# Kernel optimization log

Hardware: AMD Instinct MI355X
Metric: run time of the kernel (lower is better)

Reference implementation:

```python
import jax, jax.numpy as jnp
import numpy as np

NOISE_LEVEL = 0.05  # midpoint of uniform(0.01, 0.1) in the original
A_COEF = 0.99
B_COEF = 0.01


def setup_inputs() -> dict:
    key = jax.random.key(0)
    k1, k2 = jax.random.split(key)
    C, T = 256, 220500
    waveform = jax.random.normal(k1, (C, T), dtype=jnp.float32)
    white_noise = jax.random.normal(k2, (C, T), dtype=jnp.float32)
    return {"waveform": waveform, "white_noise": white_noise}


def _pink_noise(white_noise):
    # First-order IIR: f[0] = w[0]; f[i] = 0.99*f[i-1] + 0.01*w[i]
    # Vectorized over channels, lax.scan over time.
    w0 = white_noise[:, 0]                      # [C]
    wt = white_noise[:, 1:].T                   # [T-1, C]

    def step(carry, w_t):
        f = A_COEF * carry + B_COEF * w_t
        return f, f

    _, rest = jax.lax.scan(step, w0, wt)        # rest: [T-1, C]
    pink = jnp.concatenate([w0[None, :], rest], axis=0).T  # [C, T]
    return pink


def reference(waveform, white_noise):
    pink = _pink_noise(white_noise)
    mixed = waveform + pink * NOISE_LEVEL
    max_val = jnp.max(jnp.abs(mixed))
    # normalize only if peak exceeds 1.0
    return jnp.where(max_val > 1.0, mixed / max_val, mixed)
```

## Files before the change

### kernel.cpp

```cpp
#include <hip/hip_runtime.h>


#define TLEN 220500
#define CHANNELS 256

constexpr int CL   = 8192;
constexpr int NT   = 256;
constexpr int NSB  = 8;
constexpr int NCHUNK = (TLEN + CL - 1) / CL;
constexpr int NBLK = NCHUNK * CHANNELS;

constexpr float AC = 0.99f;
constexpr float BC = 0.01f;
constexpr float NL = 0.05f;

constexpr double dpow(double a, int n) { double r = 1.0; for (int i = 0; i < n; ++i) r *= a; return r; }

constexpr float WP0 = (float)dpow(0.99, 4 * 1);
constexpr float WP1 = (float)dpow(0.99, 4 * 2);
constexpr float WP2 = (float)dpow(0.99, 4 * 4);
constexpr float WP3 = (float)dpow(0.99, 4 * 8);
constexpr float WP4 = (float)dpow(0.99, 4 * 16);
constexpr float WP5 = (float)dpow(0.99, 4 * 32);
constexpr float A256  = (float)dpow(0.99, 256);
constexpr float A1024 = (float)dpow(0.99, 1024);
constexpr float L2A4   = -0.05799827878044602f;
constexpr float L2A256 = -3.7118898419485456f;

__global__ void init_max_kernel(unsigned int* gmax) { *gmax = 0u; }

__device__ __forceinline__ float wave_scan4(float f, int lane) {
    { float o = __shfl_up(f, 1,  64); if (lane >= 1)  f = fmaf(WP0, o, f); }
    { float o = __shfl_up(f, 2,  64); if (lane >= 2)  f = fmaf(WP1, o, f); }
    { float o = __shfl_up(f, 4,  64); if (lane >= 4)  f = fmaf(WP2, o, f); }
    { float o = __shfl_up(f, 8,  64); if (lane >= 8)  f = fmaf(WP3, o, f); }
    { float o = __shfl_up(f, 16, 64); if (lane >= 16) f = fmaf(WP4, o, f); }
    { float o = __shfl_up(f, 32, 64); if (lane >= 32) f = fmaf(WP5, o, f); }
    return f;
}

template <int USE_ATOMIC>
__global__ __launch_bounds__(NT, 4)
void pink_mix_kernel(const float* __restrict__ waveform,
                     const float* __restrict__ white,
                     float* __restrict__ out,
                     unsigned int* __restrict__ gmax,
                     float* __restrict__ blockmax)
{
    __shared__ float sB[NSB + 1][4];
    __shared__ float sM[4];
    __shared__ float sW0;

    const int chunk = blockIdx.x;
    const int ch    = blockIdx.y;
    const int c0    = chunk * CL;
    const size_t rowoff = (size_t)ch * TLEN;
    const float* __restrict__ wrow = white + rowoff;
    const float* __restrict__ arow = waveform + rowoff;
    float* __restrict__ orow = out + rowoff;

    const int tid  = threadIdx.x;
    const int lane = tid & 63;
    const int wv   = tid >> 6;

    float4 wf[NSB];
    float4 af[NSB];
    #pragma unroll
    for (int i = 0; i < NSB; ++i) {
        int g = c0 + i * 1024 + 4 * tid;
        if (g < TLEN) {
            wf[i] = *reinterpret_cast<const float4*>(wrow + g);
            af[i] = *reinterpret_cast<const float4*>(arow + g);
        } else {
            wf[i] = make_float4(0.f, 0.f, 0.f, 0.f);
            af[i] = make_float4(0.f, 0.f, 0.f, 0.f);
        }
    }
    float4 wu = make_float4(0.f, 0.f, 0.f, 0.f);
    if (chunk > 0)
        wu = *reinterpret_cast<const float4*>(wrow + (c0 - 1024) + 4 * tid);

    float eB[NSB];
    #pragma unroll
    for (int i = 0; i < NSB; ++i) {
        float f = BC * wf[i].x;
        f = fmaf(AC, f, BC * wf[i].y);
        f = fmaf(AC, f, BC * wf[i].z);
        f = fmaf(AC, f, BC * wf[i].w);
        float pB = wave_scan4(f, lane);
        float e  = __shfl_up(pB, 1, 64);
        eB[i] = (lane == 0) ? 0.f : e;
        if (lane == 63) sB[i][wv] = pB;
    }

    if (chunk > 0) {
        float f = BC * wu.x;
        f = fmaf(AC, f, BC * wu.y);
        f = fmaf(AC, f, BC * wu.z);
        f = fmaf(AC, f, BC * wu.w);
        float pB = wave_scan4(f, lane);
        if (lane == 63) sB[NSB][wv] = pB;
    }
    if (tid == 0) sW0 = wf[0].x;
    __syncthreads();

    float E;
    if (chunk > 0) {
        float t = sB[NSB][0];
        t = fmaf(A256, t, sB[NSB][1]);
        t = fmaf(A256, t, sB[NSB][2]);
        t = fmaf(A256, t, sB[NSB][3]);
        E = t;
    } else {
        E = sW0;
    }

    const float D4L = __builtin_exp2f((float)lane * L2A4);
    const float DW  = __builtin_exp2f((float)wv   * L2A256);

    float mx = 0.f;
    #pragma unroll
    for (int i = 0; i < NSB; ++i) {
        const float b0 = sB[i][0], b1 = sB[i][1], b2 = sB[i][2];
        float wB = 0.f;
        if (wv > 0) wB = b0;
        if (wv > 1) wB = fmaf(A256, wB, b1);
        if (wv > 2) wB = fmaf(A256, wB, b2);
        float f = fmaf(D4L, fmaf(DW, E, wB), eB[i]);

        int g = c0 + i * 1024 + 4 * tid;
        if (g < TLEN) {
            float4 m;
            f = fmaf(AC, f, BC * wf[i].x); m.x = fmaf(NL, f, af[i].x);
            f = fmaf(AC, f, BC * wf[i].y); m.y = fmaf(NL, f, af[i].y);
            f = fmaf(AC, f, BC * wf[i].z); m.z = fmaf(NL, f, af[i].z);
            f = fmaf(AC, f, BC * wf[i].w); m.w = fmaf(NL, f, af[i].w);
            *reinterpret_cast<float4*>(orow + g) = m;
            mx = fmaxf(mx, fmaxf(fmaxf(fabsf(m.x), fabsf(m.y)),
                                 fmaxf(fabsf(m.z), fabsf(m.w))));
        }
        float t = b0;
        t = fmaf(A256, t, b1);
        t = fmaf(A256, t, b2);
        t = fmaf(A256, t, sB[i][3]);
        E = fmaf(A1024, E, t);
    }

    #pragma unroll
    for (int d = 32; d >= 1; d >>= 1)
        mx = fmaxf(mx, __shfl_xor(mx, d, 64));
    if (lane == 0) sM[wv] = mx;
    __syncthreads();
    if (tid == 0) {
        float m = fmaxf(fmaxf(sM[0], sM[1]), fmaxf(sM[2], sM[3]));
        if (USE_ATOMIC) {
            atomicMax(gmax, __float_as_uint(m));
        } else {
            blockmax[ch * NCHUNK + chunk] = m;
        }
    }
}

__global__ __launch_bounds__(256)
void reduce_max_kernel(const float* __restrict__ blockmax, unsigned int* __restrict__ gmax)
{
    __shared__ float sM[4];
    const int tid  = threadIdx.x;
    const int lane = tid & 63;
    const int wv   = tid >> 6;
    float mx = 0.f;
    for (int i = tid; i < NBLK; i += 256)
        mx = fmaxf(mx, blockmax[i]);
    #pragma unroll
    for (int d = 32; d >= 1; d >>= 1)
        mx = fmaxf(mx, __shfl_xor(mx, d, 64));
    if (lane == 0) sM[wv] = mx;
    __syncthreads();
    if (tid == 0)
        *gmax = __float_as_uint(fmaxf(fmaxf(sM[0], sM[1]), fmaxf(sM[2], sM[3])));
}

__global__ __launch_bounds__(256)
void scale_kernel(float* __restrict__ out, const unsigned int* __restrict__ gmax, int n4)
{
    const float m = __uint_as_float(*gmax);
    const float s = (m > 1.0f) ? (1.0f / m) : 1.0f;
    float4* p = reinterpret_cast<float4*>(out);
    int i = blockIdx.x * blockDim.x + threadIdx.x;
    const int stride = gridDim.x * blockDim.x;
    for (; i < n4; i += stride) {
        float4 v = p[i];
        v.x *= s; v.y *= s; v.z *= s; v.w *= s;
        p[i] = v;
    }
}

extern "C" void kernel_launch(void* const* d_in, const int* in_sizes, int n_in,
                              void* d_out, int out_size, void* d_ws, size_t ws_size,
                              hipStream_t stream)
{
    const float* waveform = (const float*)d_in[0];
    const float* white    = (const float*)d_in[1];
    float* out            = (float*)d_out;

    unsigned int* gmax = (unsigned int*)d_ws;
    float* blockmax    = (float*)((char*)d_ws + 256);
    const bool ws_ok   = ws_size >= 256 + (size_t)NBLK * sizeof(float);

    dim3 grid(NCHUNK, CHANNELS);
    const int n4 = out_size / 4;

    if (ws_ok) {
        hipLaunchKernelGGL((pink_mix_kernel<0>), grid, dim3(NT), 0, stream,
                           waveform, white, out, gmax, blockmax);
        hipLaunchKernelGGL(reduce_max_kernel, dim3(1), dim3(256), 0, stream,
                           blockmax, gmax);
    } else {
        hipLaunchKernelGGL(init_max_kernel, dim3(1), dim3(1), 0, stream, gmax);
        hipLaunchKernelGGL((pink_mix_kernel<1>), grid, dim3(NT), 0, stream,
                           waveform, white, out, gmax, blockmax);
    }
    hipLaunchKernelGGL(scale_kernel, dim3(3072), dim3(256), 0, stream,
                       out, gmax, n4);
}
```

Before: 231.4 us.

## Replace truncated-carry chunk scan with exact three-pass segmented scan

Replaces the single fused kernel, which rebuilt each chunk's incoming IIR state from only the preceding 1024 samples, with three passes. A totals pass computes per-256-sample segment sums. A per-channel chain kernel propagates exact carries across segments. A grid-stride apply kernel then recomputes the local scan, mixes in the waveform and records block maxima. This gives an exact carry and a flat persistent grid, but it reads the white-noise array an extra full time and adds two kernel launches. The old kernel is kept as a fallback for small workspaces.

```diff
diff --git a/kernel.cpp b/kernel.cpp
--- a/kernel.cpp
+++ b/kernel.cpp
@@ -4,17 +4,18 @@
 #define TLEN 220500
 #define CHANNELS 256
 
-constexpr int CL   = 8192;
-constexpr int NT   = 256;
-constexpr int NSB  = 8;
-constexpr int NCHUNK = (TLEN + CL - 1) / CL;
-constexpr int NBLK = NCHUNK * CHANNELS;
+constexpr int SEGL = 256;
+constexpr int SPC  = (TLEN + SEGL - 1) / SEGL;
+constexpr int NSEG = SPC * CHANNELS;
+constexpr int KB   = 14;
+constexpr int GB   = 2048;
+constexpr int NBLK = GB;
 
 constexpr float AC = 0.99f;
 constexpr float BC = 0.01f;
 constexpr float NL = 0.05f;
 
-constexpr double dpow(double a, int n) { double r = 1.0; for (int i = 0; i < n; ++i) r *= a; return r; }
+constexpr double dpow(double a, long n) { double r = 1.0; for (long i = 0; i < n; ++i) r *= a; return r; }
 
 constexpr float WP0 = (float)dpow(0.99, 4 * 1);
 constexpr float WP1 = (float)dpow(0.99, 4 * 2);
@@ -22,12 +23,11 @@
 constexpr float WP3 = (float)dpow(0.99, 4 * 8);
 constexpr float WP4 = (float)dpow(0.99, 4 * 16);
 constexpr float WP5 = (float)dpow(0.99, 4 * 32);
-constexpr float A256  = (float)dpow(0.99, 256);
-constexpr float A1024 = (float)dpow(0.99, 1024);
+constexpr float A256 = (float)dpow(0.99, 256);
+constexpr float CH1 = (float)dpow(0.99, 3584);
+constexpr float CH2 = (float)dpow(0.99, 7168);
 constexpr float L2A4   = -0.05799827878044602f;
 constexpr float L2A256 = -3.7118898419485456f;
-
-__global__ void init_max_kernel(unsigned int* gmax) { *gmax = 0u; }
 
 __device__ __forceinline__ float wave_scan4(float f, int lane) {
     { float o = __shfl_up(f, 1,  64); if (lane >= 1)  f = fmaf(WP0, o, f); }
@@ -39,126 +39,116 @@
     return f;
 }
 
-template <int USE_ATOMIC>
-__global__ __launch_bounds__(NT, 4)
-void pink_mix_kernel(const float* __restrict__ waveform,
-                     const float* __restrict__ white,
-                     float* __restrict__ out,
-                     unsigned int* __restrict__ gmax,
-                     float* __restrict__ blockmax)
-{
-    __shared__ float sB[NSB + 1][4];
+__global__ __launch_bounds__(256)
+void totals_kernel(const float* __restrict__ white, float* __restrict__ totals)
+{
+    const int lane = threadIdx.x & 63;
+    const int wv   = threadIdx.x >> 6;
+    const int step = gridDim.x * 4;
+    for (int S = blockIdx.x * 4 + wv; S < NSEG; S += step) {
+        const unsigned ch = (unsigned)S / (unsigned)SPC;
+        const unsigned s  = (unsigned)S - ch * SPC;
+        const int off = (int)(s * SEGL) + 4 * lane;
+        float4 v = make_float4(0.f, 0.f, 0.f, 0.f);
+        if (off < TLEN)
+            v = *reinterpret_cast<const float4*>(white + (size_t)ch * TLEN + off);
+        float f = BC * v.x;
+        f = fmaf(AC, f, BC * v.y);
+        f = fmaf(AC, f, BC * v.z);
+        f = fmaf(AC, f, BC * v.w);
+        float p = wave_scan4(f, lane);
+        if (lane == 63) totals[S] = p;
+    }
+}
+
+__global__ __launch_bounds__(64)
+void chain_kernel(const float* __restrict__ white,
+                  const float* __restrict__ totals,
+                  float* __restrict__ Earr)
+{
+    const int ch   = blockIdx.x;
+    const int lane = threadIdx.x;
+    const float w0 = white[(size_t)ch * TLEN];
+
+    float T[KB];
+    const int sbase = lane * KB;
+    #pragma unroll
+    for (int k = 0; k < KB; ++k) {
+        int s = sbase + k;
+        T[k] = (s < SPC) ? totals[ch * SPC + s] : 0.f;
+    }
+    float B = 0.f;
+    #pragma unroll
+    for (int k = 0; k < KB; ++k) B = fmaf(A256, B, T[k]);
+    float p = B;
+    { float o = __shfl_up(p, 1, 64); if (lane >= 1) p = fmaf(CH1, o, p); }
+    { float o = __shfl_up(p, 2, 64); if (lane >= 2) p = fmaf(CH2, o, p); }
+    float X = __shfl_up(p, 1, 64);
+    if (lane == 0) X = 0.f;
+    float st = X;
+    #pragma unroll
+    for (int k = 0; k < KB; ++k) {
+        int s = sbase + k;
+        if (s < SPC)
+            Earr[ch * SPC + s] = fmaf(__builtin_exp2f((float)s * L2A256), w0, st);
+        st = fmaf(A256, st, T[k]);
+    }
+}
+
+__global__ __launch_bounds__(256)
+void apply_kernel(const float* __restrict__ waveform,
+                  const float* __restrict__ white,
+                  const float* __restrict__ Earr,
+                  float* __restrict__ out,
+                  float* __restrict__ blockmax)
+{
     __shared__ float sM[4];
-    __shared__ float sW0;
-
-    const int chunk = blockIdx.x;
-    const int ch    = blockIdx.y;
-    const int c0    = chunk * CL;
-    const size_t rowoff = (size_t)ch * TLEN;
-    const float* __restrict__ wrow = white + rowoff;
-    const float* __restrict__ arow = waveform + rowoff;
-    float* __restrict__ orow = out + rowoff;
-
-    const int tid  = threadIdx.x;
-    const int lane = tid & 63;
-    const int wv   = tid >> 6;
-
-    float4 wf[NSB];
-    float4 af[NSB];
-    #pragma unroll
-    for (int i = 0; i < NSB; ++i) {
-        int g = c0 + i * 1024 + 4 * tid;
-        if (g < TLEN) {
-            wf[i] = *reinterpret_cast<const float4*>(wrow + g);
-            af[i] = *reinterpret_cast<const float4*>(arow + g);
-        } else {
-            wf[i] = make_float4(0.f, 0.f, 0.f, 0.f);
-            af[i] = make_float4(0.f, 0.f, 0.f, 0.f);
+    const int lane = threadIdx.x & 63;
+    const int wv   = threadIdx.x >> 6;
+    const float D4L = __builtin_exp2f((float)lane * L2A4);
+    const int step = gridDim.x * 4;
+    float mx = 0.f;
+    for (int S = blockIdx.x * 4 + wv; S < NSEG; S += step) {
+        const unsigned ch = (unsigned)S / (unsigned)SPC;
+        const unsigned s  = (unsigned)S - ch * SPC;
+        const int base = (int)((size_t)0) ;
+        const int off = (int)(s * SEGL) + 4 * lane;
+        const int rowoff = (int)(ch * (unsigned)TLEN);
+        const bool ok = off < TLEN;
+        float4 wv4 = make_float4(0.f, 0.f, 0.f, 0.f);
+        float4 av4 = make_float4(0.f, 0.f, 0.f, 0.f);
+        if (ok) {
+            wv4 = *reinterpret_cast<const float4*>(white + rowoff + off);
+            av4 = *reinterpret_cast<const float4*>(waveform + rowoff + off);
         }
-    }
-    float4 wu = make_float4(0.f, 0.f, 0.f, 0.f);
-    if (chunk > 0)
-        wu = *reinterpret_cast<const float4*>(wrow + (c0 - 1024) + 4 * tid);
-
-    float eB[NSB];
-    #pragma unroll
-    for (int i = 0; i < NSB; ++i) {
-        float f = BC * wf[i].x;
-        f = fmaf(AC, f, BC * wf[i].y);
-        f = fmaf(AC, f, BC * wf[i].z);
-        f = fmaf(AC, f, BC * wf[i].w);
-        float pB = wave_scan4(f, lane);
-        float e  = __shfl_up(pB, 1, 64);
-        eB[i] = (lane == 0) ? 0.f : e;
-        if (lane == 63) sB[i][wv] = pB;
-    }
-
-    if (chunk > 0) {
-        float f = BC * wu.x;
-        f = fmaf(AC, f, BC * wu.y);
-        f = fmaf(AC, f, BC * wu.z);
-        f = fmaf(AC, f, BC * wu.w);
-        float pB = wave_scan4(f, lane);
-        if (lane == 63) sB[NSB][wv] = pB;
-    }
-    if (tid == 0) sW0 = wf[0].x;
-    __syncthreads();
-
-    float E;
-    if (chunk > 0) {
-        float t = sB[NSB][0];
-        t = fmaf(A256, t, sB[NSB][1]);
-        t = fmaf(A256, t, sB[NSB][2]);
-        t = fmaf(A256, t, sB[NSB][3]);
-        E = t;
-    } else {
-        E = sW0;
-    }
-
-    const float D4L = __builtin_exp2f((float)lane * L2A4);
-    const float DW  = __builtin_exp2f((float)wv   * L2A256);
-
-    float mx = 0.f;
-    #pragma unroll
-    for (int i = 0; i < NSB; ++i) {
-        const float b0 = sB[i][0], b1 = sB[i][1], b2 = sB[i][2];
-        float wB = 0.f;
-        if (wv > 0) wB = b0;
-        if (wv > 1) wB = fmaf(A256, wB, b1);
-        if (wv > 2) wB = fmaf(A256, wB, b2);
-        float f = fmaf(D4L, fmaf(DW, E, wB), eB[i]);
-
-        int g = c0 + i * 1024 + 4 * tid;
-        if (g < TLEN) {
-            float4 m;
-            f = fmaf(AC, f, BC * wf[i].x); m.x = fmaf(NL, f, af[i].x);
-            f = fmaf(AC, f, BC * wf[i].y); m.y = fmaf(NL, f, af[i].y);
-            f = fmaf(AC, f, BC * wf[i].z); m.z = fmaf(NL, f, af[i].z);
-            f = fmaf(AC, f, BC * wf[i].w); m.w = fmaf(NL, f, af[i].w);
-            *reinterpret_cast<float4*>(orow + g) = m;
+        const float E = Earr[S];
+        (void)base;
+        float f = BC * wv4.x;
+        f = fmaf(AC, f, BC * wv4.y);
+        f = fmaf(AC, f, BC * wv4.z);
+        f = fmaf(AC, f, BC * wv4.w);
+        float p = wave_scan4(f, lane);
+        float e = __shfl_up(p, 1, 64);
+        if (lane == 0) e = 0.f;
+        f = fmaf(D4L, E, e);
+        float4 m;
+        f = fmaf(AC, f, BC * wv4.x); m.x = fmaf(NL, f, av4.x);
+        f = fmaf(AC, f, BC * wv4.y); m.y = fmaf(NL, f, av4.y);
+        f = fmaf(AC, f, BC * wv4.z); m.z = fmaf(NL, f, av4.z);
+        f = fmaf(AC, f, BC * wv4.w); m.w = fmaf(NL, f, av4.w);
+        if (ok) {
+            *reinterpret_cast<float4*>(out + rowoff + off) = m;
             mx = fmaxf(mx, fmaxf(fmaxf(fabsf(m.x), fabsf(m.y)),
                                  fmaxf(fabsf(m.z), fabsf(m.w))));
         }
-        float t = b0;
-        t = fmaf(A256, t, b1);
-        t = fmaf(A256, t, b2);
-        t = fmaf(A256, t, sB[i][3]);
-        E = fmaf(A1024, E, t);
-    }
-
+    }
     #pragma unroll
     for (int d = 32; d >= 1; d >>= 1)
         mx = fmaxf(mx, __shfl_xor(mx, d, 64));
     if (lane == 0) sM[wv] = mx;
     __syncthreads();
-    if (tid == 0) {
-        float m = fmaxf(fmaxf(sM[0], sM[1]), fmaxf(sM[2], sM[3]));
-        if (USE_ATOMIC) {
-            atomicMax(gmax, __float_as_uint(m));
-        } else {
-            blockmax[ch * NCHUNK + chunk] = m;
-        }
-    }
+    if (threadIdx.x == 0)
+        blockmax[blockIdx.x] = fmaxf(fmaxf(sM[0], sM[1]), fmaxf(sM[2], sM[3]));
 }
 
 __global__ __launch_bounds__(256)
@@ -195,6 +185,95 @@
     }
 }
 
+__global__ void init_max_kernel(unsigned int* gmax) { *gmax = 0u; }
+
+constexpr int FCL = 8192, FNT = 256, FNSB = 8;
+constexpr int FNCHUNK = (TLEN + FCL - 1) / FCL;
+constexpr float A1024 = (float)dpow(0.99, 1024);
+
+__global__ __launch_bounds__(FNT, 4)
+void pink_mix_fallback(const float* __restrict__ waveform,
+                       const float* __restrict__ white,
+                       float* __restrict__ out,
+                       unsigned int* __restrict__ gmax)
+{
+    __shared__ float sB[FNSB + 1][4];
+    __shared__ float sM[4];
+    __shared__ float sW0;
+    const int chunk = blockIdx.x, ch = blockIdx.y, c0 = chunk * FCL;
+    const size_t rowoff = (size_t)ch * TLEN;
+    const float* wrow = white + rowoff;
+    const float* arow = waveform + rowoff;
+    float* orow = out + rowoff;
+    const int tid = threadIdx.x, lane = tid & 63, wvv = tid >> 6;
+    float4 wf[FNSB], af[FNSB];
+    #pragma unroll
+    for (int i = 0; i < FNSB; ++i) {
+        int g = c0 + i * 1024 + 4 * tid;
+        if (g < TLEN) {
+            wf[i] = *reinterpret_cast<const float4*>(wrow + g);
+            af[i] = *reinterpret_cast<const float4*>(arow + g);
+        } else { wf[i] = make_float4(0,0,0,0); af[i] = make_float4(0,0,0,0); }
+    }
+    float4 wu = make_float4(0,0,0,0);
+    if (chunk > 0) wu = *reinterpret_cast<const float4*>(wrow + (c0 - 1024) + 4 * tid);
+    float eB[FNSB];
+    #pragma unroll
+    for (int i = 0; i < FNSB; ++i) {
+        float f = BC * wf[i].x;
+        f = fmaf(AC, f, BC * wf[i].y); f = fmaf(AC, f, BC * wf[i].z); f = fmaf(AC, f, BC * wf[i].w);
+        float pB = wave_scan4(f, lane);
+        float e = __shfl_up(pB, 1, 64);
+        eB[i] = (lane == 0) ? 0.f : e;
+        if (lane == 63) sB[i][wvv] = pB;
+    }
+    if (chunk > 0) {
+        float f = BC * wu.x;
+        f = fmaf(AC, f, BC * wu.y); f = fmaf(AC, f, BC * wu.z); f = fmaf(AC, f, BC * wu.w);
+        float pB = wave_scan4(f, lane);
+        if (lane == 63) sB[FNSB][wvv] = pB;
+    }
+    if (tid == 0) sW0 = wf[0].x;
+    __syncthreads();
+    float E;
+    if (chunk > 0) {
+        float t = sB[FNSB][0];
+        t = fmaf(A256, t, sB[FNSB][1]); t = fmaf(A256, t, sB[FNSB][2]); t = fmaf(A256, t, sB[FNSB][3]);
+        E = t;
+    } else E = sW0;
+    const float D4L = __builtin_exp2f((float)lane * L2A4);
+    const float DW  = __builtin_exp2f((float)wvv  * L2A256);
+    float mx = 0.f;
+    #pragma unroll
+    for (int i = 0; i < FNSB; ++i) {
+        const float b0 = sB[i][0], b1 = sB[i][1], b2 = sB[i][2];
+        float wB = 0.f;
+        if (wvv > 0) wB = b0;
+        if (wvv > 1) wB = fmaf(A256, wB, b1);
+        if (wvv > 2) wB = fmaf(A256, wB, b2);
+        float f = fmaf(D4L, fmaf(DW, E, wB), eB[i]);
+        int g = c0 + i * 1024 + 4 * tid;
+        if (g < TLEN) {
+            float4 m;
+            f = fmaf(AC, f, BC * wf[i].x); m.x = fmaf(NL, f, af[i].x);
+            f = fmaf(AC, f, BC * wf[i].y); m.y = fmaf(NL, f, af[i].y);
+            f = fmaf(AC, f, BC * wf[i].z); m.z = fmaf(NL, f, af[i].z);
+            f = fmaf(AC, f, BC * wf[i].w); m.w = fmaf(NL, f, af[i].w);
+            *reinterpret_cast<float4*>(orow + g) = m;
+            mx = fmaxf(mx, fmaxf(fmaxf(fabsf(m.x), fabsf(m.y)), fmaxf(fabsf(m.z), fabsf(m.w))));
+        }
+        float t = b0;
+        t = fmaf(A256, t, b1); t = fmaf(A256, t, b2); t = fmaf(A256, t, sB[i][3]);
+        E = fmaf(A1024, E, t);
+    }
+    #pragma unroll
+    for (int d = 32; d >= 1; d >>= 1) mx = fmaxf(mx, __shfl_xor(mx, d, 64));
+    if (lane == 0) sM[wvv] = mx;
+    __syncthreads();
+    if (tid == 0)
+        atomicMax(gmax, __float_as_uint(fmaxf(fmaxf(sM[0], sM[1]), fmaxf(sM[2], sM[3]))));
+}
+
 extern "C" void kernel_launch(void* const* d_in, const int* in_sizes, int n_in,
                               void* d_out, int out_size, void* d_ws, size_t ws_size,
                               hipStream_t stream)
@@ -204,22 +283,25 @@
     float* out            = (float*)d_out;
 
     unsigned int* gmax = (unsigned int*)d_ws;
-    float* blockmax    = (float*)((char*)d_ws + 256);
-    const bool ws_ok   = ws_size >= 256 + (size_t)NBLK * sizeof(float);
-
-    dim3 grid(NCHUNK, CHANNELS);
+    float* blockmax = (float*)((char*)d_ws + 256);
+    const size_t off_tot = 256 + (size_t)GB * 4;
+    float* totals = (float*)((char*)d_ws + ((off_tot + 255) & ~(size_t)255));
+    float* Earr   = totals + NSEG;
+    const size_t need = ((off_tot + 255) & ~(size_t)255) + 2 * (size_t)NSEG * 4;
+
     const int n4 = out_size / 4;
 
-    if (ws_ok) {
-        hipLaunchKernelGGL((pink_mix_kernel<0>), grid, dim3(NT), 0, stream,
-                           waveform, white, out, gmax, blockmax);
-        hipLaunchKernelGGL(reduce_max_kernel, dim3(1), dim3(256), 0, stream,
-                           blockmax, gmax);
+    if (ws_size >= need) {
+        hipLaunchKernelGGL(totals_kernel, dim3(GB), dim3(256), 0, stream, white, totals);
+        hipLaunchKernelGGL(chain_kernel, dim3(CHANNELS), dim3(64), 0, stream,
+                           white, totals, Earr);
+        hipLaunchKernelGGL(apply_kernel, dim3(GB), dim3(256), 0, stream,
+                           waveform, white, Earr, out, blockmax);
+        hipLaunchKernelGGL(reduce_max_kernel, dim3(1), dim3(256), 0, stream, blockmax, gmax);
     } else {
         hipLaunchKernelGGL(init_max_kernel, dim3(1), dim3(1), 0, stream, gmax);
-        hipLaunchKernelGGL((pink_mix_kernel<1>), grid, dim3(NT), 0, stream,
-                           waveform, white, out, gmax, blockmax);
-    }
-    hipLaunchKernelGGL(scale_kernel, dim3(3072), dim3(256), 0, stream,
-                       out, gmax, n4);
-}
+        hipLaunchKernelGGL(pink_mix_fallback, dim3(FNCHUNK, CHANNELS), dim3(FNT), 0, stream,
+                           waveform, white, out, gmax);
+    }
+    hipLaunchKernelGGL(scale_kernel, dim3(3072), dim3(256), 0, stream, out, gmax, n4);
+}
```

Result: slower. 274.0 us (+18.4%).

## Assign one wave per time chunk with streamed triple-buffered loads and no block sync

Applied to the files above, without the earlier changes.

Restructures the pink-noise scan so each 64-lane wave owns a whole 8192-sample chunk of one channel. The wave walks through it in 512-sample pieces, 8 samples per lane, using a triple-buffered register prefetch two pieces ahead. This removes the shared-memory cross-wave combine and __syncthreads, and replaces the up-front load of the full chunk with streamed loads that overlap the scan arithmetic. The risk is a longer serial dependency per wave across 16 pieces and more shuffles per sample, which lowers parallelism per chunk.

```diff
diff --git a/kernel.cpp b/kernel.cpp
--- a/kernel.cpp
+++ b/kernel.cpp
@@ -4,146 +4,152 @@
 #define TLEN 220500
 #define CHANNELS 256
 
-constexpr int CL   = 8192;
-constexpr int NT   = 256;
-constexpr int NSB  = 8;
-constexpr int NCHUNK = (TLEN + CL - 1) / CL;
-constexpr int NBLK = NCHUNK * CHANNELS;
+constexpr int CHK  = 8192;
+constexpr int PL   = 512;
+constexpr int NP   = CHK / PL;
+constexpr int NCH  = 27;
+constexpr int NWAVES = NCH * CHANNELS;
+constexpr int NB   = NWAVES / 4;
 
 constexpr float AC = 0.99f;
 constexpr float BC = 0.01f;
 constexpr float NL = 0.05f;
 
-constexpr double dpow(double a, int n) { double r = 1.0; for (int i = 0; i < n; ++i) r *= a; return r; }
-
-constexpr float WP0 = (float)dpow(0.99, 4 * 1);
-constexpr float WP1 = (float)dpow(0.99, 4 * 2);
-constexpr float WP2 = (float)dpow(0.99, 4 * 4);
-constexpr float WP3 = (float)dpow(0.99, 4 * 8);
-constexpr float WP4 = (float)dpow(0.99, 4 * 16);
-constexpr float WP5 = (float)dpow(0.99, 4 * 32);
-constexpr float A256  = (float)dpow(0.99, 256);
-constexpr float A1024 = (float)dpow(0.99, 1024);
-constexpr float L2A4   = -0.05799827878044602f;
-constexpr float L2A256 = -3.7118898419485456f;
+constexpr double dpow(double a, long n) { double r = 1.0; for (long i = 0; i < n; ++i) r *= a; return r; }
+
+constexpr float S8P0 = (float)dpow(0.99, 8);
+constexpr float S8P1 = (float)dpow(0.99, 16);
+constexpr float S8P2 = (float)dpow(0.99, 32);
+constexpr float S8P3 = (float)dpow(0.99, 64);
+constexpr float S8P4 = (float)dpow(0.99, 128);
+constexpr float S8P5 = (float)dpow(0.99, 256);
+constexpr float A512 = (float)dpow(0.99, 512);
+constexpr float L2A8 = -0.11599655756609923f;
+
+__device__ __forceinline__ float wave_scan8(float f, int lane) {
+    { float o = __shfl_up(f, 1,  64); if (lane >= 1)  f = fmaf(S8P0, o, f); }
+    { float o = __shfl_up(f, 2,  64); if (lane >= 2)  f = fmaf(S8P1, o, f); }
+    { float o = __shfl_up(f, 4,  64); if (lane >= 4)  f = fmaf(S8P2, o, f); }
+    { float o = __shfl_up(f, 8,  64); if (lane >= 8)  f = fmaf(S8P3, o, f); }
+    { float o = __shfl_up(f, 16, 64); if (lane >= 16) f = fmaf(S8P4, o, f); }
+    { float o = __shfl_up(f, 32, 64); if (lane >= 32) f = fmaf(S8P5, o, f); }
+    return f;
+}
+
+__device__ __forceinline__ float serial8(const float4& a, const float4& b) {
+    float f = BC * a.x;
+    f = fmaf(AC, f, BC * a.y);
+    f = fmaf(AC, f, BC * a.z);
+    f = fmaf(AC, f, BC * a.w);
+    f = fmaf(AC, f, BC * b.x);
+    f = fmaf(AC, f, BC * b.y);
+    f = fmaf(AC, f, BC * b.z);
+    f = fmaf(AC, f, BC * b.w);
+    return f;
+}
 
 __global__ void init_max_kernel(unsigned int* gmax) { *gmax = 0u; }
 
-__device__ __forceinline__ float wave_scan4(float f, int lane) {
-    { float o = __shfl_up(f, 1,  64); if (lane >= 1)  f = fmaf(WP0, o, f); }
-    { float o = __shfl_up(f, 2,  64); if (lane >= 2)  f = fmaf(WP1, o, f); }
-    { float o = __shfl_up(f, 4,  64); if (lane >= 4)  f = fmaf(WP2, o, f); }
-    { float o = __shfl_up(f, 8,  64); if (lane >= 8)  f = fmaf(WP3, o, f); }
-    { float o = __shfl_up(f, 16, 64); if (lane >= 16) f = fmaf(WP4, o, f); }
-    { float o = __shfl_up(f, 32, 64); if (lane >= 32) f = fmaf(WP5, o, f); }
-    return f;
-}
-
 template <int USE_ATOMIC>
-__global__ __launch_bounds__(NT, 4)
-void pink_mix_kernel(const float* __restrict__ waveform,
-                     const float* __restrict__ white,
-                     float* __restrict__ out,
-                     unsigned int* __restrict__ gmax,
-                     float* __restrict__ blockmax)
-{
-    __shared__ float sB[NSB + 1][4];
+__global__ __launch_bounds__(256)
+void fused_kernel(const float* __restrict__ waveform,
+                  const float* __restrict__ white,
+                  float* __restrict__ out,
+                  unsigned int* __restrict__ gmax,
+                  float* __restrict__ blockmax)
+{
     __shared__ float sM[4];
-    __shared__ float sW0;
-
-    const int chunk = blockIdx.x;
-    const int ch    = blockIdx.y;
-    const int c0    = chunk * CL;
-    const size_t rowoff = (size_t)ch * TLEN;
-    const float* __restrict__ wrow = white + rowoff;
-    const float* __restrict__ arow = waveform + rowoff;
-    float* __restrict__ orow = out + rowoff;
-
     const int tid  = threadIdx.x;
     const int lane = tid & 63;
     const int wv   = tid >> 6;
-
-    float4 wf[NSB];
-    float4 af[NSB];
-    #pragma unroll
-    for (int i = 0; i < NSB; ++i) {
-        int g = c0 + i * 1024 + 4 * tid;
+    const int W    = blockIdx.x * 4 + wv;
+    const int ch   = W / NCH;
+    const int chunk = W - ch * NCH;
+    const size_t row = (size_t)ch * TLEN;
+    const float* __restrict__ wrow = white + row;
+    const float* __restrict__ arow = waveform + row;
+    float* __restrict__ orow = out + row;
+    const int c0 = chunk * CHK;
+    const int l8 = 8 * lane;
+    const float D8L = __builtin_exp2f((float)lane * L2A8);
+
+    float4 wu0, wu1, wu2, wu3;
+    if (chunk > 0) {
+        const float* wb = wrow + (c0 - 1024) + l8;
+        wu0 = *reinterpret_cast<const float4*>(wb);
+        wu1 = *reinterpret_cast<const float4*>(wb + 4);
+        wu2 = *reinterpret_cast<const float4*>(wb + 512);
+        wu3 = *reinterpret_cast<const float4*>(wb + 516);
+    }
+
+    float4 WA[3], WB[3], AA[3], AB[3];
+    const float4 z4 = make_float4(0.f, 0.f, 0.f, 0.f);
+
+    auto LDP = [&](int p, float4& wa, float4& wb, float4& aa, float4& ab) {
+        const int g = c0 + p * PL + l8;
+        wa = z4; wb = z4; aa = z4; ab = z4;
         if (g < TLEN) {
-            wf[i] = *reinterpret_cast<const float4*>(wrow + g);
-            af[i] = *reinterpret_cast<const float4*>(arow + g);
-        } else {
-            wf[i] = make_float4(0.f, 0.f, 0.f, 0.f);
-            af[i] = make_float4(0.f, 0.f, 0.f, 0.f);
-        }
-    }
-    float4 wu = make_float4(0.f, 0.f, 0.f, 0.f);
-    if (chunk > 0)
-        wu = *reinterpret_cast<const float4*>(wrow + (c0 - 1024) + 4 * tid);
-
-    float eB[NSB];
-    #pragma unroll
-    for (int i = 0; i < NSB; ++i) {
-        float f = BC * wf[i].x;
-        f = fmaf(AC, f, BC * wf[i].y);
-        f = fmaf(AC, f, BC * wf[i].z);
-        f = fmaf(AC, f, BC * wf[i].w);
-        float pB = wave_scan4(f, lane);
-        float e  = __shfl_up(pB, 1, 64);
-        eB[i] = (lane == 0) ? 0.f : e;
-        if (lane == 63) sB[i][wv] = pB;
-    }
-
+            wa = *reinterpret_cast<const float4*>(wrow + g);
+            aa = *reinterpret_cast<const float4*>(arow + g);
+        }
+        if (g + 4 < TLEN) {
+            wb = *reinterpret_cast<const float4*>(wrow + g + 4);
+            ab = *reinterpret_cast<const float4*>(arow + g + 4);
+        }
+    };
+
+    LDP(0, WA[0], WB[0], AA[0], AB[0]);
+    LDP(1, WA[1], WB[1], AA[1], AB[1]);
+
+    float E = 0.f;
     if (chunk > 0) {
-        float f = BC * wu.x;
-        f = fmaf(AC, f, BC * wu.y);
-        f = fmaf(AC, f, BC * wu.z);
-        f = fmaf(AC, f, BC * wu.w);
-        float pB = wave_scan4(f, lane);
-        if (lane == 63) sB[NSB][wv] = pB;
-    }
-    if (tid == 0) sW0 = wf[0].x;
-    __syncthreads();
-
-    float E;
-    if (chunk > 0) {
-        float t = sB[NSB][0];
-        t = fmaf(A256, t, sB[NSB][1]);
-        t = fmaf(A256, t, sB[NSB][2]);
-        t = fmaf(A256, t, sB[NSB][3]);
-        E = t;
+        float f = serial8(wu0, wu1);
+        float p = wave_scan8(f, lane);
+        E = __shfl(p, 63, 64);
+        f = serial8(wu2, wu3);
+        p = wave_scan8(f, lane);
+        E = fmaf(A512, E, __shfl(p, 63, 64));
     } else {
-        E = sW0;
-    }
-
-    const float D4L = __builtin_exp2f((float)lane * L2A4);
-    const float DW  = __builtin_exp2f((float)wv   * L2A256);
+        E = __shfl(WA[0].x, 0, 64);
+    }
 
     float mx = 0.f;
     #pragma unroll
-    for (int i = 0; i < NSB; ++i) {
-        const float b0 = sB[i][0], b1 = sB[i][1], b2 = sB[i][2];
-        float wB = 0.f;
-        if (wv > 0) wB = b0;
-        if (wv > 1) wB = fmaf(A256, wB, b1);
-        if (wv > 2) wB = fmaf(A256, wB, b2);
-        float f = fmaf(D4L, fmaf(DW, E, wB), eB[i]);
-
-        int g = c0 + i * 1024 + 4 * tid;
+    for (int p = 0; p < NP; ++p) {
+        const int s  = p % 3;
+        const int s2 = (p + 2) % 3;
+        if (p + 2 < NP)
+            LDP(p + 2, WA[s2], WB[s2], AA[s2], AB[s2]);
+
+        float f  = serial8(WA[s], WB[s]);
+        float pb = wave_scan8(f, lane);
+        float e  = __shfl_up(pb, 1, 64);
+        if (lane == 0) e = 0.f;
+        const float T = __shfl(pb, 63, 64);
+
+        float fst = fmaf(D8L, E, e);
+        float4 ma, mb;
+        fst = fmaf(AC, fst, BC * WA[s].x); ma.x = fmaf(NL, fst, AA[s].x);
+        fst = fmaf(AC, fst, BC * WA[s].y); ma.y = fmaf(NL, fst, AA[s].y);
+        fst = fmaf(AC, fst, BC * WA[s].z); ma.z = fmaf(NL, fst, AA[s].z);
+        fst = fmaf(AC, fst, BC * WA[s].w); ma.w = fmaf(NL, fst, AA[s].w);
+        fst = fmaf(AC, fst, BC * WB[s].x); mb.x = fmaf(NL, fst, AB[s].x);
+        fst = fmaf(AC, fst, BC * WB[s].y); mb.y = fmaf(NL, fst, AB[s].y);
+        fst = fmaf(AC, fst, BC * WB[s].z); mb.z = fmaf(NL, fst, AB[s].z);
+        fst = fmaf(AC, fst, BC * WB[s].w); mb.w = fmaf(NL, fst, AB[s].w);
+
+        const int g = c0 + p * PL + l8;
         if (g < TLEN) {
-            float4 m;
-            f = fmaf(AC, f, BC * wf[i].x); m.x = fmaf(NL, f, af[i].x);
-            f = fmaf(AC, f, BC * wf[i].y); m.y = fmaf(NL, f, af[i].y);
-            f = fmaf(AC, f, BC * wf[i].z); m.z = fmaf(NL, f, af[i].z);
-            f = fmaf(AC, f, BC * wf[i].w); m.w = fmaf(NL, f, af[i].w);
-            *reinterpret_cast<float4*>(orow + g) = m;
-            mx = fmaxf(mx, fmaxf(fmaxf(fabsf(m.x), fabsf(m.y)),
-                                 fmaxf(fabsf(m.z), fabsf(m.w))));
-        }
-        float t = b0;
-        t = fmaf(A256, t, b1);
-        t = fmaf(A256, t, b2);
-        t = fmaf(A256, t, sB[i][3]);
-        E = fmaf(A1024, E, t);
+            *reinterpret_cast<float4*>(orow + g) = ma;
+            mx = fmaxf(mx, fmaxf(fmaxf(fabsf(ma.x), fabsf(ma.y)),
+                                 fmaxf(fabsf(ma.z), fabsf(ma.w))));
+        }
+        if (g + 4 < TLEN) {
+            *reinterpret_cast<float4*>(orow + g + 4) = mb;
+            mx = fmaxf(mx, fmaxf(fmaxf(fabsf(mb.x), fabsf(mb.y)),
+                                 fmaxf(fabsf(mb.z), fabsf(mb.w))));
+        }
+        E = fmaf(A512, E, T);
     }
 
     #pragma unroll
@@ -156,7 +162,7 @@
         if (USE_ATOMIC) {
             atomicMax(gmax, __float_as_uint(m));
         } else {
-            blockmax[ch * NCHUNK + chunk] = m;
+            blockmax[blockIdx.x] = m;
         }
     }
 }
@@ -169,7 +175,7 @@
     const int lane = tid & 63;
     const int wv   = tid >> 6;
     float mx = 0.f;
-    for (int i = tid; i < NBLK; i += 256)
+    for (int i = tid; i < NB; i += 256)
         mx = fmaxf(mx, blockmax[i]);
     #pragma unroll
     for (int d = 32; d >= 1; d >>= 1)
@@ -205,19 +211,18 @@
 
     unsigned int* gmax = (unsigned int*)d_ws;
     float* blockmax    = (float*)((char*)d_ws + 256);
-    const bool ws_ok   = ws_size >= 256 + (size_t)NBLK * sizeof(float);
-
-    dim3 grid(NCHUNK, CHANNELS);
+    const bool ws_ok   = ws_size >= 256 + (size_t)NB * sizeof(float);
+
     const int n4 = out_size / 4;
 
     if (ws_ok) {
-        hipLaunchKernelGGL((pink_mix_kernel<0>), grid, dim3(NT), 0, stream,
+        hipLaunchKernelGGL((fused_kernel<0>), dim3(NB), dim3(256), 0, stream,
                            waveform, white, out, gmax, blockmax);
         hipLaunchKernelGGL(reduce_max_kernel, dim3(1), dim3(256), 0, stream,
                            blockmax, gmax);
     } else {
         hipLaunchKernelGGL(init_max_kernel, dim3(1), dim3(1), 0, stream, gmax);
-        hipLaunchKernelGGL((pink_mix_kernel<1>), grid, dim3(NT), 0, stream,
+        hipLaunchKernelGGL((fused_kernel<1>), dim3(NB), dim3(256), 0, stream,
                            waveform, white, out, gmax, blockmax);
     }
     hipLaunchKernelGGL(scale_kernel, dim3(3072), dim3(256), 0, stream,
```

Result: slower. 255.2 us (+10.3%).
